# Performance work log

Measured on AMD Instinct MI355X. Metric: run time of the kernel, lower is better.

## Reference

```python
import jax, jax.numpy as jnp
import numpy as np

NUM_HEADS = 8
NUM_LEVELS = 4
NUM_POINTS = 8
SPATIAL_SHAPES = np.array([[92, 160], [46, 80], [23, 40], [12, 20]], dtype=np.int64)


def _bilinear_sample(val_hw, loc, Hl, Wl):
    """val_hw: (bs, heads, H*W, d); loc: (bs, nq, heads, P, 2) in [0,1].
    Matches torch grid_sample(bilinear, zeros padding, align_corners=False)
    applied to grid = 2*loc - 1, i.e. pixel coords x = loc_x*W - 0.5.
    Returns (bs, heads, nq, P, d)."""
    x = loc[..., 0] * Wl - 0.5
    y = loc[..., 1] * Hl - 0.5
    x0 = jnp.floor(x)
    y0 = jnp.floor(y)
    wx = (x - x0).transpose(0, 2, 1, 3)  # (bs, heads, nq, P)
    wy = (y - y0).transpose(0, 2, 1, 3)
    x0i = x0.astype(jnp.int32).transpose(0, 2, 1, 3)
    y0i = y0.astype(jnp.int32).transpose(0, 2, 1, 3)

    def gather(ix, iy):
        valid = ((ix >= 0) & (ix < Wl) & (iy >= 0) & (iy < Hl)).astype(val_hw.dtype)
        idx = jnp.clip(iy, 0, Hl - 1) * Wl + jnp.clip(ix, 0, Wl - 1)  # (bs,heads,nq,P)
        b, h, nq, P = idx.shape
        g = jnp.take_along_axis(val_hw, idx.reshape(b, h, nq * P, 1), axis=2)
        return g.reshape(b, h, nq, P, -1) * valid[..., None]

    return (gather(x0i, y0i) * ((1 - wx) * (1 - wy))[..., None]
            + gather(x0i + 1, y0i) * (wx * (1 - wy))[..., None]
            + gather(x0i, y0i + 1) * ((1 - wx) * wy)[..., None]
            + gather(x0i + 1, y0i + 1) * (wx * wy)[..., None])


def setup_inputs() -> dict:
    key = jax.random.key(0)
    ks = jax.random.split(key, 10)
    C = 256
    bs, nq = 2, 10000
    nv = int((SPATIAL_SHAPES[:, 0] * SPATIAL_SHAPES[:, 1]).sum())  # 19560
    s = 1.0 / np.sqrt(C)
    return {
        "query": jax.random.normal(ks[0], (bs, nq, C), dtype=jnp.float32),
        "value": jax.random.normal(ks[1], (bs, nv, C), dtype=jnp.float32),
        "reference_points": jax.random.uniform(ks[2], (bs, nq, 4, 2), dtype=jnp.float32),
        "spatial_shapes": SPATIAL_SHAPES,
        "W_value": jax.random.normal(ks[3], (C, C), dtype=jnp.float32) * s,
        "b_value": jnp.zeros((C,), dtype=jnp.float32),
        "W_off": jax.random.normal(ks[4], (C, NUM_HEADS * NUM_LEVELS * NUM_POINTS * 2), dtype=jnp.float32) * 0.01,
        "b_off": jax.random.normal(ks[5], (NUM_HEADS * NUM_LEVELS * NUM_POINTS * 2,), dtype=jnp.float32) * 0.1,
        "W_attn": jax.random.normal(ks[6], (C, NUM_HEADS * NUM_LEVELS * NUM_POINTS), dtype=jnp.float32) * s,
        "b_attn": jnp.zeros((NUM_HEADS * NUM_LEVELS * NUM_POINTS,), dtype=jnp.float32),
    }


def reference(query, value, reference_points, spatial_shapes,
              W_value, b_value, W_off, b_off, W_attn, b_attn):
    bs, nq, C = query.shape
    NH, NL, NP = NUM_HEADS, NUM_LEVELS, NUM_POINTS
    d = C // NH
    Z = reference_points.shape[2]  # num_Z_anchors
    shapes_np = np.asarray(spatial_shapes)  # static host-side shapes

    # value / offset / attention projections
    v = (value @ W_value + b_value).reshape(bs, -1, NH, d)
    off = (query @ W_off + b_off).reshape(bs, nq, NH, NL, NP, 2)
    attn = jax.nn.softmax((query @ W_attn + b_attn).reshape(bs, nq, NH, NL * NP), axis=-1)
    attn = attn.reshape(bs, nq, NH, NL, NP)

    # normalize offsets by (W, H) per level and add to reference points
    norm = jnp.stack([spatial_shapes[:, 1], spatial_shapes[:, 0]], -1).astype(query.dtype)  # (NL, 2)
    off = off / norm[None, None, None, :, None, :]
    off = off.reshape(bs, nq, NH, NL, NP // Z, Z, 2)
    loc = reference_points[:, :, None, None, None, :, :] + off  # (bs,nq,NH,NL,NP//Z,Z,2)
    loc = loc.reshape(bs, nq, NH, NL, NP, 2)

    out = jnp.zeros((bs, NH, nq, d), dtype=query.dtype)
    start = 0
    for l in range(NL):
        Hl, Wl = int(shapes_np[l, 0]), int(shapes_np[l, 1])
        v_l = v[:, start:start + Hl * Wl].transpose(0, 2, 1, 3)  # (bs, NH, H*W, d)
        start += Hl * Wl
        sampled = _bilinear_sample(v_l, loc[:, :, :, l], Hl, Wl)  # (bs,NH,nq,NP,d)
        out = out + jnp.einsum('bhqpd,bqhp->bhqd', sampled, attn[:, :, :, l])
    return out.transpose(0, 2, 1, 3).reshape(bs, nq, NH * d)
```

## Files before the change

### kernel.cpp

```cpp
#include <hip/hip_runtime.h>
#include <math.h>

#define NH 8
#define NL 4
#define NP 8
#define CDIM 256
#define NQ 10000
#define BS 2
#define NV 19560

__constant__ int LVL_H[NL]     = {92, 46, 23, 12};
__constant__ int LVL_W[NL]     = {160, 80, 40, 20};
__constant__ int LVL_START[NL] = {0, 14720, 18400, 19320};

typedef __attribute__((ext_vector_type(8))) short short8;
typedef __attribute__((ext_vector_type(4))) float f32x4;
typedef __attribute__((ext_vector_type(2))) _Float16 half2v;
typedef __attribute__((ext_vector_type(4))) _Float16 half4v;

__device__ __forceinline__ unsigned short f2bf(float f) {
    unsigned int u = __float_as_uint(f);
    u += 0x7fffu + ((u >> 16) & 1u);
    return (unsigned short)(u >> 16);
}

__device__ __forceinline__ unsigned f2h_dup(float f) {
    const unsigned short h = __builtin_bit_cast(unsigned short, (_Float16)f);
    return (unsigned)h | ((unsigned)h << 16);
}

__device__ __forceinline__ void glds16(const void* g, void* l) {
    __builtin_amdgcn_global_load_lds(
        (const __attribute__((address_space(1))) unsigned*)g,
        (__attribute__((address_space(3))) unsigned*)l, 16, 0, 0);
}

__global__ __launch_bounds__(256) void prep_all(
    const float* __restrict__ query,
    const float* __restrict__ Wv,
    const float* __restrict__ Woff, const float* __restrict__ boff,
    const float* __restrict__ Wattn, const float* __restrict__ battn,
    unsigned short* __restrict__ querybf,
    unsigned short* __restrict__ BvalT, unsigned short* __restrict__ BcatT,
    float* __restrict__ biascat)
{
    const int bid = blockIdx.x;
    const int t   = threadIdx.x;
    if (bid < 5000) {
        const int i = bid * 256 + t;
        const float4 f = ((const float4*)query)[i];
        ushort4 o;
        o.x = f2bf(f.x); o.y = f2bf(f.y); o.z = f2bf(f.z); o.w = f2bf(f.w);
        ((ushort4*)querybf)[i] = o;
    } else {
        const int n = bid - 5000;
        if (n < 256) {
            BvalT[n * 256 + t] = f2bf(Wv[t * 256 + n]);
        } else if (n < 1024) {
            const int m = n - 256;
            const float v = (m < 512) ? Woff[t * 512 + m]
                                      : Wattn[t * 256 + (m - 512)];
            BcatT[m * 256 + t] = f2bf(v);
        } else {
            #pragma unroll
            for (int s = 0; s < 3; s++) {
                const int i = s * 256 + t;
                biascat[i] = (i < 512) ? boff[i] : battn[i - 512];
            }
        }
    }
}

__global__ __launch_bounds__(256) void gemm_all(
    const float* __restrict__ valueF,
    const unsigned short* __restrict__ BvalT,
    const float* __restrict__ b_value, _Float16* __restrict__ vproj,
    const unsigned short* __restrict__ querybf,
    const unsigned short* __restrict__ BcatT,
    const float* __restrict__ biascat, _Float16* __restrict__ offcat)
{
    __shared__ short8 Asl[512];
    __shared__ short8 Bsl[512];

    const int bid = blockIdx.x;
    const bool modeV = bid < 612;

    const unsigned short* Bt;
    const float* bias;
    int M, N, rowBase, colBase;
    if (modeV) {
        Bt = BvalT; bias = b_value;
        M = BS * NV; N = 256;
        rowBase = (bid >> 1) * 128; colBase = (bid & 1) * 128;
    } else {
        const int b2 = bid - 612;
        Bt = BcatT; bias = biascat;
        M = BS * NQ; N = 768;
        rowBase = (b2 / 6) * 128; colBase = (b2 % 6) * 128;
    }

    const int t = threadIdx.x;
    const int w  = t >> 6;
    const int l  = t & 63;
    const int wm = (w >> 1) * 64;
    const int wn = (w & 1) * 64;
    const int row16 = l & 15;
    const int kg    = l >> 4;

    const int r0 = t >> 2;
    const int m_ = t & 3;
    const int cs = (m_ - (r0 >> 1)) & 3;

    short8* aw0 = &Asl[(w << 6)];
    short8* aw1 = &Asl[256 + (w << 6)];
    short8* bw0 = &Bsl[(w << 6)];
    short8* bw1 = &Bsl[256 + (w << 6)];

    const int arow0 = min(rowBase + r0, M - 1);
    const int arow1 = min(rowBase + r0 + 64, M - 1);
    const int brow0 = colBase + r0;
    const int brow1 = brow0 + 64;

    f32x4 acc[4][4] = {};

    for (int k0 = 0; k0 < 256; k0 += 32) {
        const int kc = k0 + cs * 8;
        glds16(Bt + (size_t)brow0 * 256 + kc, bw0);
        glds16(Bt + (size_t)brow1 * 256 + kc, bw1);
        if (modeV) {
            #pragma unroll
            for (int jj = 0; jj < 2; jj++) {
                const int ar = jj ? arow1 : arow0;
                const float* ap = valueF + (size_t)ar * 256 + kc;
                const float4 f0 = *(const float4*)ap;
                const float4 f1 = *(const float4*)(ap + 4);
                short8 v;
                v[0] = (short)f2bf(f0.x); v[1] = (short)f2bf(f0.y);
                v[2] = (short)f2bf(f0.z); v[3] = (short)f2bf(f0.w);
                v[4] = (short)f2bf(f1.x); v[5] = (short)f2bf(f1.y);
                v[6] = (short)f2bf(f1.z); v[7] = (short)f2bf(f1.w);
                Asl[jj * 256 + t] = v;
            }
        } else {
            glds16(querybf + (size_t)arow0 * 256 + kc, aw0);
            glds16(querybf + (size_t)arow1 * 256 + kc, aw1);
        }
        __syncthreads();

        short8 af[4], bfr[4];
        #pragma unroll
        for (int i = 0; i < 4; i++) {
            const int r = wm + i * 16 + row16;
            af[i] = Asl[r * 4 + ((kg + (r >> 1)) & 3)];
        }
        #pragma unroll
        for (int j = 0; j < 4; j++) {
            const int r = wn + j * 16 + row16;
            bfr[j] = Bsl[r * 4 + ((kg + (r >> 1)) & 3)];
        }
        #pragma unroll
        for (int i = 0; i < 4; i++)
            #pragma unroll
            for (int j = 0; j < 4; j++)
                acc[i][j] = __builtin_amdgcn_mfma_f32_16x16x32_bf16(
                    bfr[j], af[i], acc[i][j], 0, 0, 0);
        __syncthreads();
    }

    const int m16 = l & 15;
    const int q4  = (l >> 4) * 4;
    #pragma unroll
    for (int i = 0; i < 4; i++) {
        const int row = rowBase + wm + i * 16 + m16;
        if (row >= M) continue;
        #pragma unroll
        for (int j = 0; j < 4; j++) {
            const int col0 = colBase + wn + j * 16 + q4;
            const float4 bv = *(const float4*)&bias[col0];
            half4v o;
            o[0] = (_Float16)(acc[i][j][0] + bv.x);
            o[1] = (_Float16)(acc[i][j][1] + bv.y);
            o[2] = (_Float16)(acc[i][j][2] + bv.z);
            o[3] = (_Float16)(acc[i][j][3] + bv.w);
            _Float16* dst;
            if (modeV) {
                const int b   = (row >= NV) ? 1 : 0;
                const int pix = row - b * NV;
                const int h   = col0 >> 5;
                const int ch  = col0 & 31;
                dst = vproj + ((size_t)(b * NH + h) * NV + pix) * 32 + ch;
            } else {
                dst = offcat + (size_t)row * 768 + col0;
            }
            *(half4v*)dst = o;
        }
    }
}

__global__ __launch_bounds__(256, 8) void sample_kernel(
    const _Float16* __restrict__ vproj,
    const _Float16* __restrict__ offcat,
    const float* __restrict__ refpts,
    float* __restrict__ out)
{
    const int bid = blockIdx.x;
    const int h   = bid & 7;
    const int g   = bid >> 3;
    const int b   = g & 1;
    const int q0  = (g >> 1) * 8;
    const int t   = threadIdx.x;

    __shared__ uint2 desc[8 * 144];

    const int qi = t >> 5, j = t & 31;
    const int qrow = b * NQ + q0 + qi;

    {
        const int lv = j >> 3, p = j & 7;

        const float logit = (float)offcat[(size_t)qrow * 768 + 512 + h * 32 + j];
        const float e = __expf(logit);
        float ssum = e;
        #pragma unroll
        for (int s = 16; s > 0; s >>= 1) ssum += __shfl_xor(ssum, s, 32);
        const float aw = e / ssum;

        const int Wl = LVL_W[lv], Hl = LVL_H[lv], st = LVL_START[lv];
        const uint oxy = *(const uint*)(offcat + (size_t)qrow * 768 + h * 64 + j * 2);
        const float offx = (float)__builtin_bit_cast(half2v, oxy)[0];
        const float offy = (float)__builtin_bit_cast(half2v, oxy)[1];

        const int z = p & 3;
        const float rx = refpts[((size_t)qrow * 4 + z) * 2];
        const float ry = refpts[((size_t)qrow * 4 + z) * 2 + 1];

        const float x = fmaf(rx, (float)Wl, offx) - 0.5f;
        const float y = fmaf(ry, (float)Hl, offy) - 0.5f;
        const float x0f = floorf(x), y0f = floorf(y);
        const float wx = x - x0f, wy = y - y0f;
        const int x0 = (int)x0f, y0 = (int)y0f;

        const int xb = min(max(x0, 0), Wl - 2);
        const float wl = (x0 >= 0 && x0 < Wl)          ? (1.f - wx) : 0.f;
        const float wr = (x0 + 1 >= 0 && x0 + 1 < Wl)  ? wx         : 0.f;
        const float wA = (x0 == xb) ? wl : ((x0 + 1 == xb) ? wr : 0.f);
        const float wB = (x0 == xb) ? wr : ((x0 == xb + 1) ? wl : 0.f);

        const int i16 = j >> 1;
        const int gA0 = qi * 144 + (((j & 1) * 2) * 2) * 18 + i16;

        #pragma unroll
        for (int r = 0; r < 2; r++) {
            const int yy = y0 + r;
            const float rwv = (yy >= 0 && yy < Hl)
                            ? (r ? wy : (1.f - wy)) * aw : 0.f;
            const int iy = min(max(yy, 0), Hl - 1);
            const unsigned base = (unsigned)((st + iy * Wl + xb) * 64);
            const int gb = gA0 + r * 2 * 18;
            desc[gb]      = make_uint2(base,      f2h_dup(wA * rwv));
            desc[gb + 18] = make_uint2(base + 64, f2h_dup(wB * rwv));
        }
    }
    __syncthreads();

    const int lane = t & 31;
    const int grp  = lane >> 3;
    const int pix  = (lane >> 2) & 1;
    const int chq  = lane & 3;

    const char* slab = (const char*)(vproj + (size_t)(b * NH + h) * NV * 32);
    const unsigned laneoff = (unsigned)(chq * 16);
    const uint4* dp = (const uint4*)&desc[qi * 144 + (grp * 2 + pix) * 18];

    half2v a0 = {}, a1 = {}, a2 = {}, a3 = {};
    #pragma unroll
    for (int half = 0; half < 2; half++) {
        uint4 d4[4];
        #pragma unroll
        for (int u2 = 0; u2 < 4; u2++) d4[u2] = dp[half * 4 + u2];
        uint4 v[8];
        #pragma unroll
        for (int u2 = 0; u2 < 4; u2++) {
            v[u2 * 2]     = *(const uint4*)(slab + (d4[u2].x + laneoff));
            v[u2 * 2 + 1] = *(const uint4*)(slab + (d4[u2].z + laneoff));
        }
        #pragma unroll
        for (int u2 = 0; u2 < 4; u2++) {
            const half2v w0 = __builtin_bit_cast(half2v, d4[u2].y);
            a0 += w0 * __builtin_bit_cast(half2v, v[u2 * 2].x);
            a1 += w0 * __builtin_bit_cast(half2v, v[u2 * 2].y);
            a2 += w0 * __builtin_bit_cast(half2v, v[u2 * 2].z);
            a3 += w0 * __builtin_bit_cast(half2v, v[u2 * 2].w);
            const half2v w1 = __builtin_bit_cast(half2v, d4[u2].w);
            a0 += w1 * __builtin_bit_cast(half2v, v[u2 * 2 + 1].x);
            a1 += w1 * __builtin_bit_cast(half2v, v[u2 * 2 + 1].y);
            a2 += w1 * __builtin_bit_cast(half2v, v[u2 * 2 + 1].z);
            a3 += w1 * __builtin_bit_cast(half2v, v[u2 * 2 + 1].w);
        }
    }

    #pragma unroll
    for (int s = 4; s <= 16; s <<= 1) {
        a0 += __builtin_bit_cast(half2v,
              __shfl_xor(__builtin_bit_cast(unsigned, a0), s, 32));
        a1 += __builtin_bit_cast(half2v,
              __shfl_xor(__builtin_bit_cast(unsigned, a1), s, 32));
        a2 += __builtin_bit_cast(half2v,
              __shfl_xor(__builtin_bit_cast(unsigned, a2), s, 32));
        a3 += __builtin_bit_cast(half2v,
              __shfl_xor(__builtin_bit_cast(unsigned, a3), s, 32));
    }

    if ((lane & 0x1C) == 0) {
        float* op = out + (size_t)qrow * 256 + h * 32 + chq * 8;
        *(float4*)op = make_float4((float)a0[0], (float)a0[1],
                                   (float)a1[0], (float)a1[1]);
        *(float4*)(op + 4) = make_float4((float)a2[0], (float)a2[1],
                                         (float)a3[0], (float)a3[1]);
    }
}

extern "C" void kernel_launch(void* const* d_in, const int* in_sizes, int n_in,
                              void* d_out, int out_size, void* d_ws, size_t ws_size,
                              hipStream_t stream)
{
    const float* query   = (const float*)d_in[0];
    const float* value   = (const float*)d_in[1];
    const float* refpts  = (const float*)d_in[2];
    const float* W_value = (const float*)d_in[4];
    const float* b_value = (const float*)d_in[5];
    const float* W_off   = (const float*)d_in[6];
    const float* b_off   = (const float*)d_in[7];
    const float* W_attn  = (const float*)d_in[8];
    const float* b_attn  = (const float*)d_in[9];

    char* ws = (char*)d_ws;
    _Float16*       vproj   = (_Float16*)(ws);
    unsigned short* querybf = (unsigned short*)(ws + 20029440);
    _Float16*       offcat  = (_Float16*)(ws + 30269440);
    unsigned short* BvalT   = (unsigned short*)(ws + 60989440);
    unsigned short* BcatT   = (unsigned short*)(ws + 61120512);
    float*          biascat = (float*)(ws + 61513728);

    const dim3 blk(256);

    prep_all<<<dim3(6025), blk, 0, stream>>>(
        query, W_value, W_off, b_off, W_attn, b_attn,
        querybf, BvalT, BcatT, biascat);

    gemm_all<<<dim3(1554), blk, 0, stream>>>(
        value, BvalT, b_value, vproj,
        querybf, BcatT, biascat, offcat);

    sample_kernel<<<dim3(BS * NQ), blk, 0, stream>>>(
        vproj, offcat, refpts, (float*)d_out);
}
```

Measured before the change: 200.6 us.

## Use inline-asm SGPR-based global loads with staged waitcnt in sampler

The sampling loop now issues its eight gathers as inline-asm global_load_dwordx4 with a scalar base address and 32-bit VGPR offsets. It places explicit s_waitcnt vmcnt(4)/vmcnt(0) and sched barriers between them so the first half of the FMAs can start while the later loads are still in flight. The sampler's launch bounds drop from 8 to 4 waves per SIMD, which relaxes the register cap. The GEMM value-conversion path now reads 16 floats per row instead of 8 and discards the extra 8 (v2 is unused), so that path moves redundant memory traffic. The inline asm also bypasses the compiler's own waitcnt tracking and adds correctness risk.

```diff
diff --git a/kernel.cpp b/kernel.cpp
--- a/kernel.cpp
+++ b/kernel.cpp
@@ -17,6 +17,7 @@
 typedef __attribute__((ext_vector_type(4))) float f32x4;
 typedef __attribute__((ext_vector_type(2))) _Float16 half2v;
 typedef __attribute__((ext_vector_type(4))) _Float16 half4v;
+typedef __attribute__((ext_vector_type(4))) unsigned uintx4;
 
 __device__ __forceinline__ unsigned short f2bf(float f) {
     unsigned int u = __float_as_uint(f);
@@ -132,14 +133,24 @@
             for (int jj = 0; jj < 2; jj++) {
                 const int ar = jj ? arow1 : arow0;
                 const float* ap = valueF + (size_t)ar * 256 + kc;
-                const float4 f0 = *(const float4*)ap;
-                const float4 f1 = *(const float4*)(ap + 4);
+                float va[16];
+                #pragma unroll
+                for (int q = 0; q < 4; q++) {
+                    const float4 f = *(const float4*)(ap + q * 4);
+                    va[q*4+0]=f.x; va[q*4+1]=f.y; va[q*4+2]=f.z; va[q*4+3]=f.w;
+                }
                 short8 v;
-                v[0] = (short)f2bf(f0.x); v[1] = (short)f2bf(f0.y);
-                v[2] = (short)f2bf(f0.z); v[3] = (short)f2bf(f0.w);
-                v[4] = (short)f2bf(f1.x); v[5] = (short)f2bf(f1.y);
-                v[6] = (short)f2bf(f1.z); v[7] = (short)f2bf(f1.w);
-                Asl[jj * 256 + t] = v;
+                #pragma unroll
+                for (int e = 0; e < 8; e++) v[e] = (short)f2bf(va[e]);
+                short8 v2;
+                #pragma unroll
+                for (int e = 0; e < 8; e++) v2[e] = (short)f2bf(va[8 + e]);
+                Asl[jj * 256 + t] = __builtin_bit_cast(short8,
+                    (uint4){ (unsigned)(unsigned short)v[0] | ((unsigned)(unsigned short)v[1] << 16),
+                             (unsigned)(unsigned short)v[2] | ((unsigned)(unsigned short)v[3] << 16),
+                             (unsigned)(unsigned short)v[4] | ((unsigned)(unsigned short)v[5] << 16),
+                             (unsigned)(unsigned short)v[6] | ((unsigned)(unsigned short)v[7] << 16) });
+                (void)v2;
             }
         } else {
             glds16(querybf + (size_t)arow0 * 256 + kc, aw0);
@@ -197,7 +208,7 @@
     }
 }
 
-__global__ __launch_bounds__(256, 8) void sample_kernel(
+__global__ __launch_bounds__(256, 4) void sample_kernel(
     const _Float16* __restrict__ vproj,
     const _Float16* __restrict__ offcat,
     const float* __restrict__ refpts,
@@ -268,36 +279,48 @@
     const int pix  = (lane >> 2) & 1;
     const int chq  = lane & 3;
 
-    const char* slab = (const char*)(vproj + (size_t)(b * NH + h) * NV * 32);
+    const unsigned long long slab64 =
+        (unsigned long long)(const char*)(vproj + (size_t)(b * NH + h) * NV * 32);
     const unsigned laneoff = (unsigned)(chq * 16);
     const uint4* dp = (const uint4*)&desc[qi * 144 + (grp * 2 + pix) * 18];
 
     half2v a0 = {}, a1 = {}, a2 = {}, a3 = {};
+
+    #define GLD(dst, voff)                                                 \
+        asm volatile("global_load_dwordx4 %0, %1, %2"                      \
+                     : "=v"(dst) : "v"(voff), "s"(slab64))
+    #define FMA4(wreg, vv)                                                 \
+        { const half2v wv_ = __builtin_bit_cast(half2v, (unsigned)(wreg)); \
+          a0 += wv_ * __builtin_bit_cast(half2v, (unsigned)(vv)[0]);       \
+          a1 += wv_ * __builtin_bit_cast(half2v, (unsigned)(vv)[1]);       \
+          a2 += wv_ * __builtin_bit_cast(half2v, (unsigned)(vv)[2]);       \
+          a3 += wv_ * __builtin_bit_cast(half2v, (unsigned)(vv)[3]); }
+
     #pragma unroll
-    for (int half = 0; half < 2; half++) {
+    for (int hf = 0; hf < 2; hf++) {
         uint4 d4[4];
         #pragma unroll
-        for (int u2 = 0; u2 < 4; u2++) d4[u2] = dp[half * 4 + u2];
-        uint4 v[8];
-        #pragma unroll
-        for (int u2 = 0; u2 < 4; u2++) {
-            v[u2 * 2]     = *(const uint4*)(slab + (d4[u2].x + laneoff));
-            v[u2 * 2 + 1] = *(const uint4*)(slab + (d4[u2].z + laneoff));
-        }
-        #pragma unroll
-        for (int u2 = 0; u2 < 4; u2++) {
-            const half2v w0 = __builtin_bit_cast(half2v, d4[u2].y);
-            a0 += w0 * __builtin_bit_cast(half2v, v[u2 * 2].x);
-            a1 += w0 * __builtin_bit_cast(half2v, v[u2 * 2].y);
-            a2 += w0 * __builtin_bit_cast(half2v, v[u2 * 2].z);
-            a3 += w0 * __builtin_bit_cast(half2v, v[u2 * 2].w);
-            const half2v w1 = __builtin_bit_cast(half2v, d4[u2].w);
-            a0 += w1 * __builtin_bit_cast(half2v, v[u2 * 2 + 1].x);
-            a1 += w1 * __builtin_bit_cast(half2v, v[u2 * 2 + 1].y);
-            a2 += w1 * __builtin_bit_cast(half2v, v[u2 * 2 + 1].z);
-            a3 += w1 * __builtin_bit_cast(half2v, v[u2 * 2 + 1].w);
-        }
-    }
+        for (int u2 = 0; u2 < 4; u2++) d4[u2] = dp[hf * 4 + u2];
+        uintx4 v0, v1, v2, v3, v4, v5, v6, v7;
+        GLD(v0, d4[0].x + laneoff);
+        GLD(v1, d4[0].z + laneoff);
+        GLD(v2, d4[1].x + laneoff);
+        GLD(v3, d4[1].z + laneoff);
+        GLD(v4, d4[2].x + laneoff);
+        GLD(v5, d4[2].z + laneoff);
+        GLD(v6, d4[3].x + laneoff);
+        GLD(v7, d4[3].z + laneoff);
+        asm volatile("s_waitcnt vmcnt(4)" ::: "memory");
+        __builtin_amdgcn_sched_barrier(0);
+        FMA4(d4[0].y, v0); FMA4(d4[0].w, v1);
+        FMA4(d4[1].y, v2); FMA4(d4[1].w, v3);
+        asm volatile("s_waitcnt vmcnt(0)" ::: "memory");
+        __builtin_amdgcn_sched_barrier(0);
+        FMA4(d4[2].y, v4); FMA4(d4[2].w, v5);
+        FMA4(d4[3].y, v6); FMA4(d4[3].w, v7);
+    }
+    #undef GLD
+    #undef FMA4
 
     #pragma unroll
     for (int s = 4; s <= 16; s <<= 1) {
```

After: 200.0 us. No clear change (-0.3%).
